# Performance work log

Hardware: AMD Instinct MI355X
Metric: run time of the kernel (lower is better)

## Reference

```python
import jax, jax.numpy as jnp
import numpy as np

K = 3          # kernel_size
PAD = 1        # padding
HEADS = 4
C = 128
K2 = K * K


def setup_inputs() -> dict:
    key = jax.random.key(0)
    k1, k2, k3, k4 = jax.random.split(key, 4)
    B, H, W = 4, 128, 128
    x = jax.random.normal(k1, (B, H, W, C), jnp.float32)
    w_qkv = jax.random.normal(k2, (K2 * K2 * HEADS, C), jnp.float32) * 0.02
    w_v = jax.random.normal(k3, (K2, C, C), jnp.float32) * np.sqrt(2.0 / (K2 * C))
    w_proj = jax.random.normal(k4, (C, C), jnp.float32) * 0.02
    return {"x": x, "w_qkv": w_qkv, "w_v": w_v, "w_proj": w_proj}


def _csa(x, w_qkv, w_v, w_proj):
    B, H, W, Cc = x.shape
    hd = Cc // HEADS
    scale = hd ** (-0.5)
    N = H * W
    # attention map: Linear(C -> k^4*heads); pool is identity for stride=1
    att = jnp.einsum('bhwc,oc->bhwo', x, w_qkv)                      # [B,H,W,81*heads]
    att = att.reshape(B, N, HEADS, K2, K2).transpose(0, 2, 1, 3, 4)  # [B,heads,N,k2,k2]
    att = jax.nn.softmax(att * scale, axis=-1)
    # unfold x into per-location 3x3 windows (patch index p = di*K + dj)
    xp = jnp.pad(x, ((0, 0), (PAD, PAD), (PAD, PAD), (0, 0)))
    patches = jnp.stack([xp[:, di:di + H, dj:dj + W, :]
                         for di in range(K) for dj in range(K)], axis=3)  # [B,H,W,k2,C]
    v = patches.reshape(B, N, K2, Cc)
    # grouped 1x1 conv == per-window-position CxC matmul
    v = jnp.einsum('pij,bnpj->bnpi', w_v, v)                          # [B,N,k2,C]
    v = v.reshape(B, N, K2, HEADS, hd).transpose(0, 3, 1, 2, 4)       # [B,heads,N,k2,hd]
    out = jnp.einsum('bhnpq,bhnqd->bhnpd', att, v)                    # [B,heads,N,k2,hd]
    # -> [B, C, k2, H, W] with channel index = head*hd + d (matches torch fold layout)
    out = out.transpose(0, 1, 4, 3, 2).reshape(B, Cc, K2, H, W)
    # fold: scatter-add overlapping patches back to (H, W)
    acc = jnp.zeros((B, Cc, H + 2 * PAD, W + 2 * PAD), x.dtype)
    p = 0
    for di in range(K):
        for dj in range(K):
            acc = acc.at[:, :, di:di + H, dj:dj + W].add(out[:, :, p])
            p += 1
    y = acc[:, :, PAD:PAD + H, PAD:PAD + W].transpose(0, 2, 3, 1)     # [B,H,W,C]
    return jnp.einsum('bhwc,oc->bhwo', y, w_proj)


def reference(x, w_qkv, w_v, w_proj):
    return _csa(x, w_qkv, w_v, w_proj)
```

## Files before the change

### kernel.cpp

```cpp
#include <hip/hip_runtime.h>


typedef short bf16x8 __attribute__((ext_vector_type(8)));
typedef float f32x4  __attribute__((ext_vector_type(4)));
typedef float v2f    __attribute__((ext_vector_type(2)));

#define SCALE 0.17677669529663687f

__device__ __forceinline__ unsigned short f2bf(float f) {
  unsigned u = __float_as_uint(f);
  u = (u + 0x7fffu + ((u >> 16) & 1u)) >> 16;
  return (unsigned short)u;
}
__device__ __forceinline__ float bf2f(unsigned short s) {
  return __uint_as_float(((unsigned)s) << 16);
}
__device__ __forceinline__ bf16x8 ld16(const unsigned short* p) {
  union { bf16x8 v; uint4 u; } r;
  r.u = *(const uint4*)p;
  return r.v;
}

__global__ __launch_bounds__(256) void cvt_kernel(const float* __restrict__ x,
                                                  const float* __restrict__ wq,
                                                  const float* __restrict__ wv,
                                                  const float* __restrict__ wp,
                                                  unsigned short* __restrict__ xb,
                                                  unsigned short* __restrict__ wqb,
                                                  unsigned short* __restrict__ wvb,
                                                  unsigned short* __restrict__ wpb) {
  long i = ((long)blockIdx.x * 256 + threadIdx.x) * 4;
  if (i >= 8593920) return;
  const float* src; unsigned short* dst; long off;
  if (i < 8388608)      { src = x;  dst = xb;  off = i; }
  else if (i < 8430080) { src = wq; dst = wqb; off = i - 8388608; }
  else if (i < 8577536) { src = wv; dst = wvb; off = i - 8430080; }
  else                  { src = wp; dst = wpb; off = i - 8577536; }
  float4 v = *(const float4*)(src + off);
  ushort4 o;
  o.x = f2bf(v.x); o.y = f2bf(v.y); o.z = f2bf(v.z); o.w = f2bf(v.w);
  *(ushort4*)(dst + off) = o;
}

__global__ __launch_bounds__(256) void att_kernel(const unsigned short* __restrict__ xb,
                                                  const unsigned short* __restrict__ wqb,
                                                  unsigned* __restrict__ attb) {
  __shared__ unsigned short A[64 * 136];
  __shared__ unsigned short Bl[96 * 136];
  __shared__ float lg[64][84];
  const int t = threadIdx.x;
  const long m0 = (long)blockIdx.x * 64;
  for (int i = t; i < 1024; i += 256) {
    int row = i >> 4, seg = i & 15;
    const uint4 v = *(const uint4*)(xb + (m0 + row) * 128 + seg * 8);
    *(uint4*)((unsigned*)A + row * 68 + seg * 4) = v;
  }
  const int wv = t >> 6, lane = t & 63, qd = lane >> 4, l15 = lane & 15;
  __syncthreads();
  bf16x8 af[4];
#pragma unroll
  for (int kk = 0; kk < 4; kk++)
    af[kk] = ld16(A + (wv * 16 + l15) * 136 + kk * 32 + qd * 8);

  unsigned short* attile = Bl;
  for (int h = 0; h < 4; h++) {
    __syncthreads();
    for (int i = t; i < 1296; i += 256) {
      int row = i >> 4, seg = i & 15;
      const uint4 v = *(const uint4*)(wqb + (long)(h * 81 + row) * 128 + seg * 8);
      *(uint4*)((unsigned*)Bl + row * 68 + seg * 4) = v;
    }
    __syncthreads();
    f32x4 acc[6] = {};
#pragma unroll
    for (int kk = 0; kk < 4; kk++)
#pragma unroll
      for (int tn = 0; tn < 6; tn++) {
        bf16x8 bf = ld16(Bl + (tn * 16 + l15) * 136 + kk * 32 + qd * 8);
        acc[tn] = __builtin_amdgcn_mfma_f32_16x16x32_bf16(af[kk], bf, acc[tn], 0, 0, 0);
      }
#pragma unroll
    for (int tn = 0; tn < 6; tn++)
#pragma unroll
      for (int r = 0; r < 4; r++) {
        int col = tn * 16 + l15;
        if (col < 81) lg[wv * 16 + qd * 4 + r][col] = acc[tn][r];
      }
    __syncthreads();
    for (int g = t; g < 576; g += 256) {
      int row = g / 9, p = g % 9;
      const float* L = &lg[row][p * 9];
      float mx = L[0];
#pragma unroll
      for (int q = 1; q < 9; q++) mx = fmaxf(mx, L[q]);
      float e[9], s = 0.f;
#pragma unroll
      for (int q = 0; q < 9; q++) { e[q] = __expf((L[q] - mx) * SCALE); s += e[q]; }
      float inv = 1.f / s;
#pragma unroll
      for (int q = 0; q < 9; q++) attile[row * 90 + q * 10 + p] = f2bf(e[q] * inv);
    }
    __syncthreads();
#pragma unroll
    for (int k = 0; k < 12; k++) {
      int i = t + k * 256;
      if (i < 2880) {
        int q = i / 320, rem = i - q * 320, n = rem / 5, j = rem - n * 5;
        attb[((size_t)(q * 4 + h) * 65536 + m0 + n) * 5 + j] =
            ((const unsigned*)attile)[n * 45 + q * 5 + j];
      }
    }
  }
}

__global__ __launch_bounds__(256, 2) void av_kernel(const unsigned short* __restrict__ xb,
                                                    const unsigned short* __restrict__ wvb,
                                                    const unsigned* __restrict__ attb,
                                                    const unsigned short* __restrict__ wpb,
                                                    float* __restrict__ out) {
  __shared__ unsigned short A[144 * 136];
  __shared__ unsigned short S[100 * 136];
  __shared__ unsigned aLs[2400];
  const int t = threadIdx.x;
  const int bb = blockIdx.z;
  const int r0 = blockIdx.y * 8, c0 = blockIdx.x * 8;
  const int l15 = t & 15, qd = (t >> 4) & 3, wvi = t >> 6;
  const int n = wvi * 16 + l15, lr = n >> 3, lc = n & 7;
  const long nb = (long)bb * 16384;
  unsigned* Sdw = (unsigned*)S;
  unsigned* Adw = (unsigned*)A;

  int mlr_[7], mlc_[7];
#pragma unroll
  for (int nt = 0; nt < 7; nt++) {
    int ml = nt * 16 + l15;
    mlr_[nt] = ml / 10; mlc_[nt] = ml % 10;
  }

#pragma unroll
  for (int k = 0; k < 9; k++) {
    int i = t + k * 256;
    int row = i >> 4, seg = i & 15;
    int gr = r0 - 2 + row / 12, gc = c0 - 2 + row % 12;
    uint4 v = make_uint4(0, 0, 0, 0);
    if (gr >= 0 && gr < 128 && gc >= 0 && gc < 128)
      v = *(const uint4*)(xb + (nb + gr * 128 + gc) * 128 + seg * 8);
    *(uint4*)(Adw + row * 68 + seg * 4) = v;
  }

  v2f y2[16];
#pragma unroll
  for (int i = 0; i < 16; i++) y2[i] = (v2f){0.f, 0.f};

  unsigned avv[8];
  bf16x8 wvf[2][4];

#define LOAD_A(qq)                                                                        \
  {                                                                                       \
    _Pragma("unroll") for (int k = 0; k < 8; k++) {                                       \
      int i = t + k * 256;                                                                \
      if (i < 2000) {                                                                     \
        int hh = i / 500, rem = i - hh * 500, row = rem / 5, j5 = rem - row * 5;          \
        int gr = r0 - 1 + row / 10, gc = c0 - 1 + row % 10;                               \
        avv[k] = (gr >= 0 && gr < 128 && gc >= 0 && gc < 128)                             \
                     ? attb[((size_t)((qq) * 4 + hh) * 65536 + nb + gr * 128 + gc) * 5 +  \
                            j5]                                                           \
                     : 0u;                                                                \
      }                                                                                   \
    }                                                                                     \
  }
#define LOAD_WV(qq)                                                                       \
  {                                                                                       \
    _Pragma("unroll") for (int m = 0; m < 2; m++)                                         \
    _Pragma("unroll") for (int kk = 0; kk < 4; kk++)                                      \
      wvf[m][kk] = *(const bf16x8*)(wvb + ((size_t)(qq) * 128 + (wvi * 2 + m) * 16 +      \
                                           l15) * 128 + kk * 32 + qd * 8);                \
  }

  LOAD_A(0)
  LOAD_WV(0)

  for (int q = 0; q < 9; q++) {
    const int oqr = q / 3 - 1, oqc = q % 3 - 1;
    __syncthreads();

#pragma unroll
    for (int k = 0; k < 8; k++) {
      int i = t + k * 256;
      if (i < 2000) {
        int hh = i / 500, rem = i - hh * 500, row = rem / 5, j5 = rem - row * 5;
        aLs[hh * 600 + row * 6 + j5] = avv[k];
      }
    }

    f32x4 acc[2][7];
#pragma unroll
    for (int m = 0; m < 2; m++)
#pragma unroll
      for (int nt = 0; nt < 7; nt++) acc[m][nt] = (f32x4){0.f, 0.f, 0.f, 0.f};
#pragma unroll
    for (int nt = 0; nt < 7; nt++) {
      int xr = (mlr_[nt] + oqr + 1) * 12 + (mlc_[nt] + oqc + 1);
      xr = xr > 143 ? 143 : xr;
      bf16x8 bx[4];
#pragma unroll
      for (int kk = 0; kk < 4; kk++)
        bx[kk] = ld16(A + xr * 136 + kk * 32 + qd * 8);
#pragma unroll
      for (int m = 0; m < 2; m++)
#pragma unroll
        for (int kk = 0; kk < 4; kk++)
          acc[m][nt] = __builtin_amdgcn_mfma_f32_16x16x32_bf16(wvf[m][kk], bx[kk],
                                                               acc[m][nt], 0, 0, 0);
    }
#pragma unroll
    for (int m = 0; m < 2; m++)
#pragma unroll
      for (int nt = 0; nt < 7; nt++) {
        int loc = nt * 16 + l15;
        if (loc < 100) {
          int mt = wvi * 2 + m;
          unsigned u0 = (unsigned)f2bf(acc[m][nt][0]) | ((unsigned)f2bf(acc[m][nt][1]) << 16);
          unsigned u1 = (unsigned)f2bf(acc[m][nt][2]) | ((unsigned)f2bf(acc[m][nt][3]) << 16);
          *(uint2*)(Sdw + loc * 68 + mt * 8 + qd * 2) = make_uint2(u0, u1);
        }
      }
    __syncthreads();
    if (q < 8) { LOAD_A(q + 1) LOAD_WV(q + 1) }

    const unsigned short* aS = (const unsigned short*)aLs;
#pragma unroll
    for (int p = 0; p < 9; p++) {
      const int em = 1 - p / 3, ec = 1 - p % 3;
      const int ml = (lr + em + 1) * 10 + (lc + ec + 1);
      const float a = bf2f(aS[qd * 1200 + ml * 12 + p]);
      const v2f a2 = {a, a};
      const uint4* Sr = (const uint4*)(Sdw + ml * 68 + (qd << 4));
#pragma unroll
      for (int v4 = 0; v4 < 4; v4++) {
        const uint4 u = Sr[v4];
        v2f xv;
        const int yi = v4 * 4;
        xv.x = __uint_as_float(u.x << 16); xv.y = __uint_as_float(u.x & 0xffff0000u);
        y2[yi + 0] += a2 * xv;
        xv.x = __uint_as_float(u.y << 16); xv.y = __uint_as_float(u.y & 0xffff0000u);
        y2[yi + 1] += a2 * xv;
        xv.x = __uint_as_float(u.z << 16); xv.y = __uint_as_float(u.z & 0xffff0000u);
        y2[yi + 2] += a2 * xv;
        xv.x = __uint_as_float(u.w << 16); xv.y = __uint_as_float(u.w & 0xffff0000u);
        y2[yi + 3] += a2 * xv;
      }
    }
  }

  __syncthreads();
  unsigned short* yb = A;
  {
    uint4 pk[4];
#pragma unroll
    for (int v4 = 0; v4 < 4; v4++) {
      pk[v4].x = (unsigned)f2bf(y2[v4 * 4 + 0].x) | ((unsigned)f2bf(y2[v4 * 4 + 0].y) << 16);
      pk[v4].y = (unsigned)f2bf(y2[v4 * 4 + 1].x) | ((unsigned)f2bf(y2[v4 * 4 + 1].y) << 16);
      pk[v4].z = (unsigned)f2bf(y2[v4 * 4 + 2].x) | ((unsigned)f2bf(y2[v4 * 4 + 2].y) << 16);
      pk[v4].w = (unsigned)f2bf(y2[v4 * 4 + 3].x) | ((unsigned)f2bf(y2[v4 * 4 + 3].y) << 16);
    }
    uint4* dst = (uint4*)(Adw + n * 68 + (qd << 4));
#pragma unroll
    for (int v4 = 0; v4 < 4; v4++) dst[v4] = pk[v4];
  }
  __syncthreads();
  f32x4 pacc[8] = {};
#pragma unroll
  for (int kk = 0; kk < 4; kk++) {
    bf16x8 afr = ld16(yb + (wvi * 16 + l15) * 136 + kk * 32 + qd * 8);
#pragma unroll
    for (int tn = 0; tn < 8; tn++) {
      bf16x8 bfr = *(const bf16x8*)(wpb + (tn * 16 + l15) * 128 + kk * 32 + qd * 8);
      pacc[tn] = __builtin_amdgcn_mfma_f32_16x16x32_bf16(afr, bfr, pacc[tn], 0, 0, 0);
    }
  }
#pragma unroll
  for (int tn = 0; tn < 8; tn++)
#pragma unroll
    for (int r = 0; r < 4; r++) {
      int nl = wvi * 16 + qd * 4 + r;
      int col = tn * 16 + l15;
      out[(nb + (r0 + (nl >> 3)) * 128 + (c0 + (nl & 7))) * 128 + col] = pacc[tn][r];
    }
}

extern "C" void kernel_launch(void* const* d_in, const int* in_sizes, int n_in,
                              void* d_out, int out_size, void* d_ws, size_t ws_size,
                              hipStream_t stream) {
  const float* x  = (const float*)d_in[0];
  const float* wq = (const float*)d_in[1];
  const float* wv = (const float*)d_in[2];
  const float* wp = (const float*)d_in[3];
  char* w = (char*)d_ws;
  unsigned short* xb   = (unsigned short*)w;
  unsigned*       attb = (unsigned*)(w + 16777216);
  unsigned short* wqb  = (unsigned short*)(w + 63963136);
  unsigned short* wvb  = wqb + 41472;
  unsigned short* wpb  = wvb + 147456;

  cvt_kernel<<<8393, 256, 0, stream>>>(x, wq, wv, wp, xb, wqb, wvb, wpb);
  att_kernel<<<1024, 256, 0, stream>>>(xb, wqb, attb);
  dim3 g3(16, 16, 4);
  av_kernel<<<g3, 256, 0, stream>>>(xb, wvb, attb, wpb, (float*)d_out);
}
```

Baseline: 216.3 us.

## Fuse fp32-to-bf16 conversion of x into consumer kernels, use perm-based packing

Drops the separate pass that converts x to bf16 in global memory. The attention and AV kernels now read fp32 x directly and convert while staging into shared memory, saving a 32MB read plus 16MB write and re-read. AV's halo tile means x is read at twice the width, and rounding switches to a cheaper add-and-permute pack that rounds ties away from zero rather than to even. The weight conversion kernel shrinks to cover only the weights.

```diff
diff --git a/kernel.cpp b/kernel.cpp
--- a/kernel.cpp
+++ b/kernel.cpp
@@ -15,34 +15,36 @@
 __device__ __forceinline__ float bf2f(unsigned short s) {
   return __uint_as_float(((unsigned)s) << 16);
 }
+__device__ __forceinline__ unsigned pk2bf(float lo, float hi) {
+  unsigned a = __float_as_uint(lo) + 0x8000u;
+  unsigned b = __float_as_uint(hi) + 0x8000u;
+  return __builtin_amdgcn_perm(b, a, 0x07060302u);
+}
 __device__ __forceinline__ bf16x8 ld16(const unsigned short* p) {
   union { bf16x8 v; uint4 u; } r;
   r.u = *(const uint4*)p;
   return r.v;
 }
 
-__global__ __launch_bounds__(256) void cvt_kernel(const float* __restrict__ x,
-                                                  const float* __restrict__ wq,
+__global__ __launch_bounds__(256) void cvt_kernel(const float* __restrict__ wq,
                                                   const float* __restrict__ wv,
                                                   const float* __restrict__ wp,
-                                                  unsigned short* __restrict__ xb,
                                                   unsigned short* __restrict__ wqb,
                                                   unsigned short* __restrict__ wvb,
                                                   unsigned short* __restrict__ wpb) {
   long i = ((long)blockIdx.x * 256 + threadIdx.x) * 4;
-  if (i >= 8593920) return;
+  if (i >= 205312) return;
   const float* src; unsigned short* dst; long off;
-  if (i < 8388608)      { src = x;  dst = xb;  off = i; }
-  else if (i < 8430080) { src = wq; dst = wqb; off = i - 8388608; }
-  else if (i < 8577536) { src = wv; dst = wvb; off = i - 8430080; }
-  else                  { src = wp; dst = wpb; off = i - 8577536; }
+  if (i < 41472)       { src = wq; dst = wqb; off = i; }
+  else if (i < 188928) { src = wv; dst = wvb; off = i - 41472; }
+  else                 { src = wp; dst = wpb; off = i - 188928; }
   float4 v = *(const float4*)(src + off);
   ushort4 o;
   o.x = f2bf(v.x); o.y = f2bf(v.y); o.z = f2bf(v.z); o.w = f2bf(v.w);
   *(ushort4*)(dst + off) = o;
 }
 
-__global__ __launch_bounds__(256) void att_kernel(const unsigned short* __restrict__ xb,
+__global__ __launch_bounds__(256) void att_kernel(const float* __restrict__ x,
                                                   const unsigned short* __restrict__ wqb,
                                                   unsigned* __restrict__ attb) {
   __shared__ unsigned short A[64 * 136];
@@ -50,10 +52,13 @@
   __shared__ float lg[64][84];
   const int t = threadIdx.x;
   const long m0 = (long)blockIdx.x * 64;
-  for (int i = t; i < 1024; i += 256) {
-    int row = i >> 4, seg = i & 15;
-    const uint4 v = *(const uint4*)(xb + (m0 + row) * 128 + seg * 8);
-    *(uint4*)((unsigned*)A + row * 68 + seg * 4) = v;
+#pragma unroll
+  for (int k = 0; k < 8; k++) {
+    int i = t + k * 256;
+    int row = i >> 5, seg = i & 31;
+    float4 v = *(const float4*)(x + (m0 + row) * 128 + seg * 4);
+    *(uint2*)((unsigned*)A + row * 68 + seg * 2) =
+        make_uint2(pk2bf(v.x, v.y), pk2bf(v.z, v.w));
   }
   const int wv = t >> 6, lane = t & 63, qd = lane >> 4, l15 = lane & 15;
   __syncthreads();
@@ -113,7 +118,7 @@
   }
 }
 
-__global__ __launch_bounds__(256, 2) void av_kernel(const unsigned short* __restrict__ xb,
+__global__ __launch_bounds__(256, 2) void av_kernel(const float* __restrict__ x,
                                                     const unsigned short* __restrict__ wvb,
                                                     const unsigned* __restrict__ attb,
                                                     const unsigned short* __restrict__ wpb,
@@ -138,14 +143,14 @@
   }
 
 #pragma unroll
-  for (int k = 0; k < 9; k++) {
+  for (int k = 0; k < 18; k++) {
     int i = t + k * 256;
-    int row = i >> 4, seg = i & 15;
+    int row = i >> 5, seg = i & 31;
     int gr = r0 - 2 + row / 12, gc = c0 - 2 + row % 12;
-    uint4 v = make_uint4(0, 0, 0, 0);
+    float4 v = make_float4(0.f, 0.f, 0.f, 0.f);
     if (gr >= 0 && gr < 128 && gc >= 0 && gc < 128)
-      v = *(const uint4*)(xb + (nb + gr * 128 + gc) * 128 + seg * 8);
-    *(uint4*)(Adw + row * 68 + seg * 4) = v;
+      v = *(const float4*)(x + (nb + gr * 128 + gc) * 128 + seg * 4);
+    *(uint2*)(Adw + row * 68 + seg * 2) = make_uint2(pk2bf(v.x, v.y), pk2bf(v.z, v.w));
   }
 
   v2f y2[16];
@@ -220,9 +225,9 @@
         int loc = nt * 16 + l15;
         if (loc < 100) {
           int mt = wvi * 2 + m;
-          unsigned u0 = (unsigned)f2bf(acc[m][nt][0]) | ((unsigned)f2bf(acc[m][nt][1]) << 16);
-          unsigned u1 = (unsigned)f2bf(acc[m][nt][2]) | ((unsigned)f2bf(acc[m][nt][3]) << 16);
-          *(uint2*)(Sdw + loc * 68 + mt * 8 + qd * 2) = make_uint2(u0, u1);
+          *(uint2*)(Sdw + loc * 68 + mt * 8 + qd * 2) =
+              make_uint2(pk2bf(acc[m][nt][0], acc[m][nt][1]),
+                         pk2bf(acc[m][nt][2], acc[m][nt][3]));
         }
       }
     __syncthreads();
@@ -259,10 +264,10 @@
     uint4 pk[4];
 #pragma unroll
     for (int v4 = 0; v4 < 4; v4++) {
-      pk[v4].x = (unsigned)f2bf(y2[v4 * 4 + 0].x) | ((unsigned)f2bf(y2[v4 * 4 + 0].y) << 16);
-      pk[v4].y = (unsigned)f2bf(y2[v4 * 4 + 1].x) | ((unsigned)f2bf(y2[v4 * 4 + 1].y) << 16);
-      pk[v4].z = (unsigned)f2bf(y2[v4 * 4 + 2].x) | ((unsigned)f2bf(y2[v4 * 4 + 2].y) << 16);
-      pk[v4].w = (unsigned)f2bf(y2[v4 * 4 + 3].x) | ((unsigned)f2bf(y2[v4 * 4 + 3].y) << 16);
+      pk[v4].x = pk2bf(y2[v4 * 4 + 0].x, y2[v4 * 4 + 0].y);
+      pk[v4].y = pk2bf(y2[v4 * 4 + 1].x, y2[v4 * 4 + 1].y);
+      pk[v4].z = pk2bf(y2[v4 * 4 + 2].x, y2[v4 * 4 + 2].y);
+      pk[v4].w = pk2bf(y2[v4 * 4 + 3].x, y2[v4 * 4 + 3].y);
     }
     uint4* dst = (uint4*)(Adw + n * 68 + (qd << 4));
 #pragma unroll
@@ -297,14 +302,13 @@
   const float* wv = (const float*)d_in[2];
   const float* wp = (const float*)d_in[3];
   char* w = (char*)d_ws;
-  unsigned short* xb   = (unsigned short*)w;
-  unsigned*       attb = (unsigned*)(w + 16777216);
-  unsigned short* wqb  = (unsigned short*)(w + 63963136);
+  unsigned*       attb = (unsigned*)w;
+  unsigned short* wqb  = (unsigned short*)(w + 47185920);
   unsigned short* wvb  = wqb + 41472;
   unsigned short* wpb  = wvb + 147456;
 
-  cvt_kernel<<<8393, 256, 0, stream>>>(x, wq, wv, wp, xb, wqb, wvb, wpb);
-  att_kernel<<<1024, 256, 0, stream>>>(xb, wqb, attb);
+  cvt_kernel<<<201, 256, 0, stream>>>(wq, wv, wp, wqb, wvb, wpb);
+  att_kernel<<<1024, 256, 0, stream>>>(x, wqb, attb);
   dim3 g3(16, 16, 4);
-  av_kernel<<<g3, 256, 0, stream>>>(xb, wvb, attb, wpb, (float*)d_out);
-}
+  av_kernel<<<g3, 256, 0, stream>>>(x, wvb, attb, wpb, (float*)d_out);
+}
```

New measurement: 214.8 us. Within noise of the previous version (-0.7%).
